# Kernel optimization log

Measured on AMD Instinct MI355X. Metric: run time of the kernel, lower is better.

The kernel has to match this reference:

```python
import jax, jax.numpy as jnp
import numpy as np

N_NODES = 325
C = 64
BATCH = 64
SEQ = 12
K = 3


def setup_inputs() -> dict:
    key = jax.random.key(0)
    k1, k2, k3 = jax.random.split(key, 3)
    x = jax.random.normal(k1, (BATCH, C, N_NODES, SEQ), dtype=jnp.float32)
    # sparse-ish binary adjacency with self loops (typical traffic graph density)
    a = (jax.random.uniform(k2, (N_NODES, N_NODES)) < 0.05).astype(jnp.float32)
    adj = jnp.maximum(a, a.T)
    adj = adj.at[jnp.arange(N_NODES), jnp.arange(N_NODES)].set(1.0)
    W = jax.random.normal(k3, (K, C, C), dtype=jnp.float32) * (1.0 / np.sqrt(C))
    b = jnp.zeros((C,), dtype=jnp.float32)
    return {"x": x, "adj": adj, "W": W, "b": b}


def reference(x, adj, W, b):
    B, c_in, N, T = x.shape
    # [B, C, N, T] -> [B*T, N, C]
    xr = jnp.transpose(x, (0, 3, 2, 1)).reshape(-1, N, c_in)
    # symmetric normalized Laplacian L = I - D^{-1/2} A D^{-1/2}
    d = adj.sum(axis=-1)
    d_inv_sqrt = jnp.where(d > 0, jax.lax.rsqrt(d), 0.0)
    norm_adj = d_inv_sqrt[:, None] * adj * d_inv_sqrt[None, :]
    L = jnp.eye(N, dtype=adj.dtype) - norm_adj
    # Chebyshev recursion, K=3
    Tx0 = xr
    Tx1 = jnp.einsum('ij,bjc->bic', L, Tx0)
    out = jnp.einsum('bnc,cd->bnd', Tx0, W[0]) + jnp.einsum('bnc,cd->bnd', Tx1, W[1])
    Tx2 = 2.0 * jnp.einsum('ij,bjc->bic', L, Tx1) - Tx0
    out = out + jnp.einsum('bnc,cd->bnd', Tx2, W[2]) + b
    # [B*T, N, C] -> [B, C, N, T]
    out = out.reshape(B, T, N, c_in)
    return jnp.transpose(out, (0, 3, 2, 1))
```

## Files before the change

kernel.cpp:

```cpp
#include <hip/hip_runtime.h>
#include <hip/hip_bf16.h>

#define NND   325
#define SEQ   12
#define NT    3900
#define KP    352
#define NC    11
#define CHUNK_SHORTS 12288
#define MROWS 48

typedef __attribute__((ext_vector_type(8))) short short8;
typedef __attribute__((ext_vector_type(4))) float floatx4;

static __device__ __forceinline__ unsigned short f2bf(float f) {
    unsigned int u = __float_as_uint(f);
    unsigned int r = (u + 0x7fffu + ((u >> 16) & 1u)) >> 16;
    return (unsigned short)r;
}

static __device__ __forceinline__ int xi(int m, int j) {
    int slot = (j >> 3) ^ ((m >> 1) & 3);
    return m * KP + slot * 8 + (j & 7);
}
static __device__ __forceinline__ int swz(int n) {
    return ((n & 7) ^ ((n >> 3) & 7)) << 4;
}

__global__ void calc_dis(const float* __restrict__ adj, float* __restrict__ dis) {
    int i = blockIdx.x;
    const float* row = adj + (size_t)i * NND;
    float s = 0.f;
    for (int j = threadIdx.x; j < NND; j += 64) s += row[j];
    for (int o = 32; o; o >>= 1) s += __shfl_down(s, o);
    if (threadIdx.x == 0) dis[i] = (s > 0.f) ? rsqrtf(s) : 0.f;
}

__global__ void build_L2(const float* __restrict__ adj, const float* __restrict__ dis,
                         unsigned short* __restrict__ Lg2) {
    int s = blockIdx.x * 256 + threadIdx.x;
    if (s >= NC * CHUNK_SHORTS) return;
    int c = s / CHUNK_SHORTS, r = s - c * CHUNK_SHORTS;
    int n = r >> 5, w = r & 31;
    int j = c * 32 + w;
    float v = 0.f;
    if (n < NND && j < NND) {
        float a = adj[(size_t)n * NND + j];
        v = ((n == j) ? 1.f : 0.f) - dis[n] * a * dis[j];
    }
    Lg2[s] = f2bf(v);
}

__global__ void build_wswz(const float* __restrict__ W, unsigned short* __restrict__ wswz) {
    int idx = blockIdx.x * 256 + threadIdx.x;
    if (idx >= 64 * 192) return;
    int d = idx / 192, k = idx - d * 192;
    int kind = k >> 6, c = k & 63;
    float wv = W[kind * 4096 + c * 64 + d];
    float w;
    if (kind == 0)      w = wv - W[2 * 4096 + c * 64 + d];
    else if (kind == 1) w = wv;
    else                w = 2.f * wv;
    int byte = d * 384 + ((2 * k) ^ swz(d));
    wswz[byte >> 1] = f2bf(w);
}

__global__ __launch_bounds__(512, 2) void cheb_mfma(
        const float* __restrict__ x,
        const unsigned short* __restrict__ Lg2,
        unsigned short* __restrict__ Yg,
        unsigned short* __restrict__ Zg) {
    __shared__ __align__(16) unsigned short Xs[MROWS * KP];
    __shared__ __align__(16) unsigned short Ys[MROWS * KP];

    const int tid = threadIdx.x;
    int bid = blockIdx.x;
    bid = (bid & 7) * 128 + (bid >> 3);
    const int g0 = bid * 4;

    const int w  = tid >> 6;
    const int l  = tid & 63;
    const int lm = l & 15, lg = l >> 4;
    const int ap = (lm >> 1) & 3;

    short8 Lf[3][NC];
    #pragma unroll
    for (int i = 0; i < 3; ++i) {
        const int nrow = (w * 3 + i) * 16 + lm;
        #pragma unroll
        for (int c = 0; c < NC; ++c)
            Lf[i][c] = *(const short8*)(Lg2 + (size_t)c * CHUNK_SHORTS + nrow * 32 + lg * 8);
    }

    for (int i = tid; i < MROWS * 27; i += 512) {
        int m = i / 27, j = 325 + (i - (i / 27) * 27);
        Xs[xi(m, j)] = 0;
    }
    const float4* xb = (const float4*)(x + (size_t)g0 * NT);
    for (int i = tid; i < 3900; i += 512) {
        float4 v = xb[i];
        int f = i * 4;
        int gl = f / NT;
        int rem = f - gl * NT;
        int j = rem / SEQ;
        int t0 = rem - j * SEQ;
        int m = gl * SEQ + t0;
        Xs[xi(m + 0, j)] = f2bf(v.x);
        Xs[xi(m + 1, j)] = f2bf(v.y);
        Xs[xi(m + 2, j)] = f2bf(v.z);
        Xs[xi(m + 3, j)] = f2bf(v.w);
    }
    __syncthreads();

    floatx4 acc[3][3];

    auto zero_acc = [&]() {
        #pragma unroll
        for (int a = 0; a < 3; ++a)
            #pragma unroll
            for (int b2 = 0; b2 < 3; ++b2) acc[a][b2] = (floatx4){0.f, 0.f, 0.f, 0.f};
    };

    auto gemm = [&](const unsigned short* Aimg) {
        #pragma unroll
        for (int c = 0; c < NC; ++c) {
            short8 af[3];
            #pragma unroll
            for (int mt = 0; mt < 3; ++mt) {
                int m = mt * 16 + lm;
                int slot = (c * 4 + lg) ^ ap;
                af[mt] = *(const short8*)&Aimg[m * KP + slot * 8];
            }
            #pragma unroll
            for (int i = 0; i < 3; ++i)
                #pragma unroll
                for (int mt = 0; mt < 3; ++mt)
                    acc[mt][i] = __builtin_amdgcn_mfma_f32_16x16x32_bf16(
                        af[mt], Lf[i][c], acc[mt][i], 0, 0, 0);
        }
    };

    auto store_acc = [&](unsigned short* img) {
        #pragma unroll
        for (int i = 0; i < 3; ++i) {
            int n = (w * 3 + i) * 16 + lm;
            if (n < KP) {
                #pragma unroll
                for (int mt = 0; mt < 3; ++mt)
                    #pragma unroll
                    for (int r = 0; r < 4; ++r)
                        img[xi(mt * 16 + lg * 4 + r, n)] = f2bf(acc[mt][i][r]);
            }
        }
    };

    auto copy_out = [&](const unsigned short* img, unsigned short* dst) {
        for (int i = tid; i < 1950 * 2; i += 512) {
            int gl = i / 975;
            int r2 = i - gl * 975;
            int n = r2 / 3;
            int tq = (r2 - n * 3) * 4;
            int m = gl * SEQ + tq;
            ushort4 u;
            u.x = img[xi(m + 0, n)];
            u.y = img[xi(m + 1, n)];
            u.z = img[xi(m + 2, n)];
            u.w = img[xi(m + 3, n)];
            *(ushort4*)&dst[(size_t)(g0 + gl) * NT + n * SEQ + tq] = u;
        }
    };

    zero_acc();
    gemm(Xs);
    store_acc(Ys);
    __syncthreads();
    copy_out(Ys, Yg);

    zero_acc();
    gemm(Ys);
    store_acc(Xs);
    __syncthreads();
    copy_out(Xs, Zg);
}

__global__ __launch_bounds__(256) void mix_mfma(
        const float* __restrict__ x,
        const unsigned short* __restrict__ Yg,
        const unsigned short* __restrict__ Zg,
        const unsigned short* __restrict__ wswz,
        const float* __restrict__ bias,
        float* __restrict__ out) {
    __shared__ unsigned short Bl[96 * 192];
    __shared__ unsigned short Al[64 * 192];
    const int tid = threadIdx.x;
    int lin = blockIdx.x;
    lin = (lin & 7) * 328 + (lin >> 3);
    const int b = lin / 41;
    const int nt0 = (lin - b * 41) * 96;
    const bool tail = (nt0 + 96 > NT);

    for (int i = tid; i < 1536; i += 256)
        *(short8*)((char*)Al + i * 16) = *(const short8*)((const char*)wswz + i * 16);

    for (int i = tid; i < 768; i += 256) {
        int r = i / 12, ch = i - r * 12;
        int nt = nt0 + ch * 8;
        const float* sp = x + ((size_t)b * 64 + r) * NT + nt;
        float f[8];
        if (!tail || nt + 8 <= NT) {
            float4 v0 = *(const float4*)sp;
            float4 v1 = *(const float4*)(sp + 4);
            f[0] = v0.x; f[1] = v0.y; f[2] = v0.z; f[3] = v0.w;
            f[4] = v1.x; f[5] = v1.y; f[6] = v1.z; f[7] = v1.w;
        } else {
            #pragma unroll
            for (int jj = 0; jj < 8; ++jj) f[jj] = (nt + jj < NT) ? sp[jj] : 0.f;
        }
        int k2 = 2 * r;
        #pragma unroll
        for (int jj = 0; jj < 8; ++jj) {
            int n = ch * 8 + jj;
            *(unsigned short*)((char*)Bl + n * 384 + (k2 ^ swz(n))) = f2bf(f[jj]);
        }
    }
    for (int i = tid; i < 1536; i += 256) {
        int r = 64 + i / 12, ch = i % 12;
        int nt = nt0 + ch * 8;
        const unsigned short* base = (r < 128) ? Yg : Zg;
        const unsigned short* sp = base + ((size_t)b * 64 + (r & 63)) * NT + nt;
        unsigned short f[8];
        if (!tail || nt + 8 <= NT) {
            ushort4 v0 = *(const ushort4*)sp;
            ushort4 v1 = *(const ushort4*)(sp + 4);
            f[0] = v0.x; f[1] = v0.y; f[2] = v0.z; f[3] = v0.w;
            f[4] = v1.x; f[5] = v1.y; f[6] = v1.z; f[7] = v1.w;
        } else {
            #pragma unroll
            for (int jj = 0; jj < 8; ++jj) f[jj] = (nt + jj < NT) ? sp[jj] : (unsigned short)0;
        }
        int k2 = 2 * r;
        #pragma unroll
        for (int jj = 0; jj < 8; ++jj) {
            int n = ch * 8 + jj;
            *(unsigned short*)((char*)Bl + n * 384 + (k2 ^ swz(n))) = f[jj];
        }
    }
    __syncthreads();

    const int w = __builtin_amdgcn_readfirstlane(tid >> 6);
    const int l = tid & 63;
    const int lm = l & 15, lg = l >> 4;

    floatx4 acc[6];
    #pragma unroll
    for (int i = 0; i < 6; ++i) acc[i] = (floatx4){0.f, 0.f, 0.f, 0.f};

    const int arow = w * 16 + lm;
    const char* Ab = (const char*)Al + arow * 384;
    #pragma unroll
    for (int ks = 0; ks < 6; ++ks) {
        const int k2 = (ks * 32 + lg * 8) * 2;
        short8 a = *(const short8*)(Ab + (k2 ^ swz(arow)));
        #pragma unroll
        for (int ni = 0; ni < 6; ++ni) {
            int n = ni * 16 + lm;
            short8 bb = *(const short8*)((const char*)Bl + n * 384 + (k2 ^ swz(n)));
            acc[ni] = __builtin_amdgcn_mfma_f32_16x16x32_bf16(a, bb, acc[ni], 0, 0, 0);
        }
    }

    float br[4];
    #pragma unroll
    for (int j = 0; j < 4; ++j) br[j] = bias[w * 16 + lg * 4 + j];
    #pragma unroll
    for (int ni = 0; ni < 6; ++ni) {
        int nt = nt0 + ni * 16 + lm;
        if (nt < NT) {
            float* op = out + ((size_t)b * 64 + w * 16 + lg * 4) * NT + nt;
            #pragma unroll
            for (int j = 0; j < 4; ++j) op[(size_t)j * NT] = acc[ni][j] + br[j];
        }
    }
}

extern "C" void kernel_launch(void* const* d_in, const int* in_sizes, int n_in,
                              void* d_out, int out_size, void* d_ws, size_t ws_size,
                              hipStream_t stream) {
    const float* x   = (const float*)d_in[0];
    const float* adj = (const float*)d_in[1];
    const float* W   = (const float*)d_in[2];
    const float* b   = (const float*)d_in[3];
    float* out = (float*)d_out;

    char* ws = (char*)d_ws;
    float* dis           = (float*)(ws + 0);
    unsigned short* Lg2  = (unsigned short*)(ws + 1312);
    unsigned short* wswz = (unsigned short*)(ws + 271648);
    unsigned short* Yg   = (unsigned short*)(ws + 296224);
    unsigned short* Zg   = (unsigned short*)(ws + 32245024);

    calc_dis<<<NND, 64, 0, stream>>>(adj, dis);
    build_L2<<<(NC * CHUNK_SHORTS + 255) / 256, 256, 0, stream>>>(adj, dis, Lg2);
    build_wswz<<<48, 256, 0, stream>>>(W, wswz);
    cheb_mfma<<<1024, 512, 0, stream>>>(x, Lg2, Yg, Zg);
    mix_mfma<<<2624, 256, 0, stream>>>(x, Yg, Zg, wswz, b, out);
}
```

Measured before the change: 127.4 us.

## Split Chebyshev recursion into transpose plus two global-memory MFMA passes

Replaces the fused LDS-resident Chebyshev kernel with a transpose kernel that writes bf16 x in a [g][t][node] layout, then two separate cheb_pass launches. Each pass streams L and the source operand straight from global memory into MFMA fragments, with no shared memory and higher occupancy. The mix kernel now reads the new transposed Y/Z layout and loads the weight fragments directly from global memory instead of staging them in LDS. This removes LDS staging and block-level syncs, at the cost of an extra launch, a full round trip of the intermediate through global memory, and reliance on cache for the L and operand reuse.

```diff
diff --git a/kernel.cpp b/kernel.cpp
--- a/kernel.cpp
+++ b/kernel.cpp
@@ -4,10 +4,13 @@
 #define NND   325
 #define SEQ   12
 #define NT    3900
-#define KP    352
+#define NROW  328
+#define GROW  3936
+#define GROWB 7872
+#define TROWB 656
 #define NC    11
 #define CHUNK_SHORTS 12288
-#define MROWS 48
+#define CHUNK_BYTES  24576
 
 typedef __attribute__((ext_vector_type(8))) short short8;
 typedef __attribute__((ext_vector_type(4))) float floatx4;
@@ -16,14 +19,6 @@
     unsigned int u = __float_as_uint(f);
     unsigned int r = (u + 0x7fffu + ((u >> 16) & 1u)) >> 16;
     return (unsigned short)r;
-}
-
-static __device__ __forceinline__ int xi(int m, int j) {
-    int slot = (j >> 3) ^ ((m >> 1) & 3);
-    return m * KP + slot * 8 + (j & 7);
-}
-static __device__ __forceinline__ int swz(int n) {
-    return ((n & 7) ^ ((n >> 3) & 7)) << 4;
 }
 
 __global__ void calc_dis(const float* __restrict__ adj, float* __restrict__ dis) {
@@ -50,7 +45,7 @@
     Lg2[s] = f2bf(v);
 }
 
-__global__ void build_wswz(const float* __restrict__ W, unsigned short* __restrict__ wswz) {
+__global__ void build_w2(const float* __restrict__ W, unsigned short* __restrict__ wflat) {
     int idx = blockIdx.x * 256 + threadIdx.x;
     if (idx >= 64 * 192) return;
     int d = idx / 192, k = idx - d * 192;
@@ -60,193 +55,160 @@
     if (kind == 0)      w = wv - W[2 * 4096 + c * 64 + d];
     else if (kind == 1) w = wv;
     else                w = 2.f * wv;
-    int byte = d * 384 + ((2 * k) ^ swz(d));
-    wswz[byte >> 1] = f2bf(w);
-}
-
-__global__ __launch_bounds__(512, 2) void cheb_mfma(
-        const float* __restrict__ x,
+    wflat[idx] = f2bf(w);
+}
+
+__global__ __launch_bounds__(256) void tx_kernel(const float* __restrict__ x,
+                                                 unsigned short* __restrict__ Xt) {
+    int u = blockIdx.x * 256 + threadIdx.x;
+    int g = u / 246;
+    int r = u - g * 246;
+    int jq = r / 3, tq = r - (r / 3) * 3;
+    int j0 = jq * 4, t0 = tq * 4;
+    float a[4][4];
+    #pragma unroll
+    for (int rr = 0; rr < 4; ++rr) {
+        int j = j0 + rr;
+        if (j < NND) {
+            float4 v = *(const float4*)(x + (size_t)g * NT + j * SEQ + t0);
+            a[rr][0] = v.x; a[rr][1] = v.y; a[rr][2] = v.z; a[rr][3] = v.w;
+        } else {
+            a[rr][0] = a[rr][1] = a[rr][2] = a[rr][3] = 0.f;
+        }
+    }
+    unsigned short* dst = Xt + (size_t)g * GROW + j0;
+    #pragma unroll
+    for (int s = 0; s < 4; ++s) {
+        ushort4 o;
+        o.x = f2bf(a[0][s]); o.y = f2bf(a[1][s]);
+        o.z = f2bf(a[2][s]); o.w = f2bf(a[3][s]);
+        *(ushort4*)(dst + (size_t)(t0 + s) * NROW) = o;
+    }
+}
+
+__global__ __launch_bounds__(256, 3) void cheb_pass(
+        const unsigned short* __restrict__ src,
         const unsigned short* __restrict__ Lg2,
-        unsigned short* __restrict__ Yg,
-        unsigned short* __restrict__ Zg) {
-    __shared__ __align__(16) unsigned short Xs[MROWS * KP];
-    __shared__ __align__(16) unsigned short Ys[MROWS * KP];
-
+        unsigned short* __restrict__ dst) {
+    int bid = blockIdx.x;
+    bid = (bid & 7) * 112 + (bid >> 3);
     const int tid = threadIdx.x;
-    int bid = blockIdx.x;
-    bid = (bid & 7) * 128 + (bid >> 3);
-    const int g0 = bid * 4;
-
-    const int w  = tid >> 6;
-    const int l  = tid & 63;
-    const int lm = l & 15, lg = l >> 4;
-    const int ap = (lm >> 1) & 3;
-
-    short8 Lf[3][NC];
+    const int wid = bid * 4 + (tid >> 6);
+    const int colgrp = wid & 511;
+    const int ntri   = wid >> 9;
+    const int l = tid & 63, lm = l & 15, lg = l >> 4;
+    const int g0 = colgrp * 8;
+
+    const char* sbase = (const char*)src
+        + (size_t)(g0 + (lm & 7)) * GROWB + (lm >> 3) * TROWB + lg * 16;
+    const char* lbase[3];
     #pragma unroll
     for (int i = 0; i < 3; ++i) {
-        const int nrow = (w * 3 + i) * 16 + lm;
-        #pragma unroll
-        for (int c = 0; c < NC; ++c)
-            Lf[i][c] = *(const short8*)(Lg2 + (size_t)c * CHUNK_SHORTS + nrow * 32 + lg * 8);
-    }
-
-    for (int i = tid; i < MROWS * 27; i += 512) {
-        int m = i / 27, j = 325 + (i - (i / 27) * 27);
-        Xs[xi(m, j)] = 0;
-    }
-    const float4* xb = (const float4*)(x + (size_t)g0 * NT);
-    for (int i = tid; i < 3900; i += 512) {
-        float4 v = xb[i];
-        int f = i * 4;
-        int gl = f / NT;
-        int rem = f - gl * NT;
-        int j = rem / SEQ;
-        int t0 = rem - j * SEQ;
-        int m = gl * SEQ + t0;
-        Xs[xi(m + 0, j)] = f2bf(v.x);
-        Xs[xi(m + 1, j)] = f2bf(v.y);
-        Xs[xi(m + 2, j)] = f2bf(v.z);
-        Xs[xi(m + 3, j)] = f2bf(v.w);
-    }
-    __syncthreads();
-
-    floatx4 acc[3][3];
-
-    auto zero_acc = [&]() {
-        #pragma unroll
-        for (int a = 0; a < 3; ++a)
-            #pragma unroll
-            for (int b2 = 0; b2 < 3; ++b2) acc[a][b2] = (floatx4){0.f, 0.f, 0.f, 0.f};
-    };
-
-    auto gemm = [&](const unsigned short* Aimg) {
-        #pragma unroll
-        for (int c = 0; c < NC; ++c) {
-            short8 af[3];
-            #pragma unroll
-            for (int mt = 0; mt < 3; ++mt) {
-                int m = mt * 16 + lm;
-                int slot = (c * 4 + lg) ^ ap;
-                af[mt] = *(const short8*)&Aimg[m * KP + slot * 8];
+        int nrow = (ntri * 3 + i) * 16 + lm;
+        lbase[i] = (const char*)Lg2 + nrow * 64 + lg * 16;
+    }
+
+    floatx4 acc[3][6];
+    #pragma unroll
+    for (int i = 0; i < 3; ++i)
+        #pragma unroll
+        for (int ct = 0; ct < 6; ++ct) acc[i][ct] = (floatx4){0.f, 0.f, 0.f, 0.f};
+
+    for (int c = 0; c < NC; ++c) {
+        short8 lf[3];
+        #pragma unroll
+        for (int i = 0; i < 3; ++i)
+            lf[i] = *(const short8*)(lbase[i] + c * CHUNK_BYTES);
+        short8 df[6];
+        #pragma unroll
+        for (int ct = 0; ct < 6; ++ct)
+            df[ct] = *(const short8*)(sbase + ct * (2 * TROWB) + c * 64);
+        #pragma unroll
+        for (int i = 0; i < 3; ++i)
+            #pragma unroll
+            for (int ct = 0; ct < 6; ++ct)
+                acc[i][ct] = __builtin_amdgcn_mfma_f32_16x16x32_bf16(
+                    lf[i], df[ct], acc[i][ct], 0, 0, 0);
+    }
+
+    const int gl = lm & 7;
+    #pragma unroll
+    for (int i = 0; i < 3; ++i) {
+        int n0 = (ntri * 3 + i) * 16 + lg * 4;
+        if (n0 < NROW) {
+            #pragma unroll
+            for (int ct = 0; ct < 6; ++ct) {
+                int t = ct * 2 + (lm >> 3);
+                ushort4 o;
+                o.x = f2bf(acc[i][ct][0]); o.y = f2bf(acc[i][ct][1]);
+                o.z = f2bf(acc[i][ct][2]); o.w = f2bf(acc[i][ct][3]);
+                *(ushort4*)((char*)dst + (size_t)(g0 + gl) * GROWB + t * TROWB + n0 * 2) = o;
             }
-            #pragma unroll
-            for (int i = 0; i < 3; ++i)
-                #pragma unroll
-                for (int mt = 0; mt < 3; ++mt)
-                    acc[mt][i] = __builtin_amdgcn_mfma_f32_16x16x32_bf16(
-                        af[mt], Lf[i][c], acc[mt][i], 0, 0, 0);
-        }
-    };
-
-    auto store_acc = [&](unsigned short* img) {
-        #pragma unroll
-        for (int i = 0; i < 3; ++i) {
-            int n = (w * 3 + i) * 16 + lm;
-            if (n < KP) {
-                #pragma unroll
-                for (int mt = 0; mt < 3; ++mt)
-                    #pragma unroll
-                    for (int r = 0; r < 4; ++r)
-                        img[xi(mt * 16 + lg * 4 + r, n)] = f2bf(acc[mt][i][r]);
-            }
-        }
-    };
-
-    auto copy_out = [&](const unsigned short* img, unsigned short* dst) {
-        for (int i = tid; i < 1950 * 2; i += 512) {
-            int gl = i / 975;
-            int r2 = i - gl * 975;
-            int n = r2 / 3;
-            int tq = (r2 - n * 3) * 4;
-            int m = gl * SEQ + tq;
-            ushort4 u;
-            u.x = img[xi(m + 0, n)];
-            u.y = img[xi(m + 1, n)];
-            u.z = img[xi(m + 2, n)];
-            u.w = img[xi(m + 3, n)];
-            *(ushort4*)&dst[(size_t)(g0 + gl) * NT + n * SEQ + tq] = u;
-        }
-    };
-
-    zero_acc();
-    gemm(Xs);
-    store_acc(Ys);
-    __syncthreads();
-    copy_out(Ys, Yg);
-
-    zero_acc();
-    gemm(Ys);
-    store_acc(Xs);
-    __syncthreads();
-    copy_out(Xs, Zg);
-}
-
-__global__ __launch_bounds__(256) void mix_mfma(
+        }
+    }
+}
+
+__global__ __launch_bounds__(256) void mix2(
         const float* __restrict__ x,
         const unsigned short* __restrict__ Yg,
         const unsigned short* __restrict__ Zg,
-        const unsigned short* __restrict__ wswz,
+        const unsigned short* __restrict__ wflat,
         const float* __restrict__ bias,
         float* __restrict__ out) {
-    __shared__ unsigned short Bl[96 * 192];
-    __shared__ unsigned short Al[64 * 192];
+    __shared__ __align__(16) unsigned char Bl[96 * 400];
     const int tid = threadIdx.x;
     int lin = blockIdx.x;
     lin = (lin & 7) * 328 + (lin >> 3);
     const int b = lin / 41;
-    const int nt0 = (lin - b * 41) * 96;
-    const bool tail = (nt0 + 96 > NT);
-
-    for (int i = tid; i < 1536; i += 256)
-        *(short8*)((char*)Al + i * 16) = *(const short8*)((const char*)wswz + i * 16);
-
-    for (int i = tid; i < 768; i += 256) {
-        int r = i / 12, ch = i - r * 12;
-        int nt = nt0 + ch * 8;
-        const float* sp = x + ((size_t)b * 64 + r) * NT + nt;
-        float f[8];
-        if (!tail || nt + 8 <= NT) {
-            float4 v0 = *(const float4*)sp;
-            float4 v1 = *(const float4*)(sp + 4);
-            f[0] = v0.x; f[1] = v0.y; f[2] = v0.z; f[3] = v0.w;
-            f[4] = v1.x; f[5] = v1.y; f[6] = v1.z; f[7] = v1.w;
+    const int tile = lin - b * 41;
+    const int nt0 = tile * 96;
+    const int nn0 = tile * 8;
+
+    for (int i = tid; i < 576; i += 256) {
+        int kk = i / 192;
+        int r2 = i - kk * 192;
+        int cq = r2 / 12;
+        int tc = r2 - cq * 12;
+        int k0 = kk * 64 + cq * 4;
+        unsigned short hv[4][8];
+        if (kk == 0) {
+            int nt = nt0 + tc * 8;
+            #pragma unroll
+            for (int r = 0; r < 4; ++r) {
+                const float* sp = x + ((size_t)b * 64 + cq * 4 + r) * NT + nt;
+                float4 v0 = (nt <= NT - 4) ? *(const float4*)sp : make_float4(0.f,0.f,0.f,0.f);
+                float4 v1 = (nt <= NT - 8) ? *(const float4*)(sp + 4) : make_float4(0.f,0.f,0.f,0.f);
+                hv[r][0] = f2bf(v0.x); hv[r][1] = f2bf(v0.y);
+                hv[r][2] = f2bf(v0.z); hv[r][3] = f2bf(v0.w);
+                hv[r][4] = f2bf(v1.x); hv[r][5] = f2bf(v1.y);
+                hv[r][6] = f2bf(v1.z); hv[r][7] = f2bf(v1.w);
+            }
         } else {
-            #pragma unroll
-            for (int jj = 0; jj < 8; ++jj) f[jj] = (nt + jj < NT) ? sp[jj] : 0.f;
-        }
-        int k2 = 2 * r;
+            const unsigned short* base = (kk == 1) ? Yg : Zg;
+            #pragma unroll
+            for (int r = 0; r < 4; ++r) {
+                short8 s = *(const short8*)(base + ((size_t)b * 64 + cq * 4 + r) * GROW
+                                            + tc * NROW + nn0);
+                hv[r][0] = (unsigned short)s[0]; hv[r][1] = (unsigned short)s[1];
+                hv[r][2] = (unsigned short)s[2]; hv[r][3] = (unsigned short)s[3];
+                hv[r][4] = (unsigned short)s[4]; hv[r][5] = (unsigned short)s[5];
+                hv[r][6] = (unsigned short)s[6]; hv[r][7] = (unsigned short)s[7];
+            }
+        }
+        const int slot = k0 >> 3;
+        const int half = (k0 & 4) << 1;
         #pragma unroll
         for (int jj = 0; jj < 8; ++jj) {
-            int n = ch * 8 + jj;
-            *(unsigned short*)((char*)Bl + n * 384 + (k2 ^ swz(n))) = f2bf(f[jj]);
-        }
-    }
-    for (int i = tid; i < 1536; i += 256) {
-        int r = 64 + i / 12, ch = i % 12;
-        int nt = nt0 + ch * 8;
-        const unsigned short* base = (r < 128) ? Yg : Zg;
-        const unsigned short* sp = base + ((size_t)b * 64 + (r & 63)) * NT + nt;
-        unsigned short f[8];
-        if (!tail || nt + 8 <= NT) {
-            ushort4 v0 = *(const ushort4*)sp;
-            ushort4 v1 = *(const ushort4*)(sp + 4);
-            f[0] = v0.x; f[1] = v0.y; f[2] = v0.z; f[3] = v0.w;
-            f[4] = v1.x; f[5] = v1.y; f[6] = v1.z; f[7] = v1.w;
-        } else {
-            #pragma unroll
-            for (int jj = 0; jj < 8; ++jj) f[jj] = (nt + jj < NT) ? sp[jj] : (unsigned short)0;
-        }
-        int k2 = 2 * r;
-        #pragma unroll
-        for (int jj = 0; jj < 8; ++jj) {
-            int n = ch * 8 + jj;
-            *(unsigned short*)((char*)Bl + n * 384 + (k2 ^ swz(n))) = f[jj];
+            int q = (kk == 0) ? (tc * 8 + jj) : (jj * 12 + tc);
+            int sl = (slot & ~3) | ((slot & 3) ^ ((q >> 3) & 3));
+            ushort4 o;
+            o.x = hv[0][jj]; o.y = hv[1][jj]; o.z = hv[2][jj]; o.w = hv[3][jj];
+            *(ushort4*)(Bl + q * 400 + sl * 16 + half) = o;
         }
     }
     __syncthreads();
 
-    const int w = __builtin_amdgcn_readfirstlane(tid >> 6);
+    const int w = tid >> 6;
     const int l = tid & 63;
     const int lm = l & 15, lg = l >> 4;
 
@@ -255,15 +217,14 @@
     for (int i = 0; i < 6; ++i) acc[i] = (floatx4){0.f, 0.f, 0.f, 0.f};
 
     const int arow = w * 16 + lm;
-    const char* Ab = (const char*)Al + arow * 384;
+    const unsigned short* Ab = wflat + arow * 192;
     #pragma unroll
     for (int ks = 0; ks < 6; ++ks) {
-        const int k2 = (ks * 32 + lg * 8) * 2;
-        short8 a = *(const short8*)(Ab + (k2 ^ swz(arow)));
+        short8 a = *(const short8*)(Ab + ks * 32 + lg * 8);
         #pragma unroll
         for (int ni = 0; ni < 6; ++ni) {
-            int n = ni * 16 + lm;
-            short8 bb = *(const short8*)((const char*)Bl + n * 384 + (k2 ^ swz(n)));
+            int q = ni * 16 + lm;
+            short8 bb = *(const short8*)(Bl + q * 400 + (4 * ks + (lg ^ ((q >> 3) & 3))) * 16);
             acc[ni] = __builtin_amdgcn_mfma_f32_16x16x32_bf16(a, bb, acc[ni], 0, 0, 0);
         }
     }
@@ -294,13 +255,15 @@
     char* ws = (char*)d_ws;
     float* dis           = (float*)(ws + 0);
     unsigned short* Lg2  = (unsigned short*)(ws + 1312);
-    unsigned short* wswz = (unsigned short*)(ws + 271648);
+    unsigned short* wflat= (unsigned short*)(ws + 271648);
     unsigned short* Yg   = (unsigned short*)(ws + 296224);
-    unsigned short* Zg   = (unsigned short*)(ws + 32245024);
+    unsigned short* XtZ  = (unsigned short*)(ws + 32539936);
 
     calc_dis<<<NND, 64, 0, stream>>>(adj, dis);
     build_L2<<<(NC * CHUNK_SHORTS + 255) / 256, 256, 0, stream>>>(adj, dis, Lg2);
-    build_wswz<<<48, 256, 0, stream>>>(W, wswz);
-    cheb_mfma<<<1024, 512, 0, stream>>>(x, Lg2, Yg, Zg);
-    mix_mfma<<<2624, 256, 0, stream>>>(x, Yg, Zg, wswz, b, out);
-}
+    build_w2<<<48, 256, 0, stream>>>(W, wflat);
+    tx_kernel<<<3936, 256, 0, stream>>>(x, XtZ);
+    cheb_pass<<<896, 256, 0, stream>>>(XtZ, Lg2, Yg);
+    cheb_pass<<<896, 256, 0, stream>>>(Yg, Lg2, XtZ);
+    mix2<<<2624, 256, 0, stream>>>(x, Yg, XtZ, wflat, b, out);
+}
```

After: 260.5 us. 105% more time.
